# Kernel optimization log

Measured on AMD Instinct MI355X. Metric: run time of the kernel, lower is better.

The kernel has to match this reference:

```python
import jax, jax.numpy as jnp
import numpy as np

NEG_SLOPE = 0.2

def setup_inputs() -> dict:
    key = jax.random.key(0)
    k1, k2, k3, k4, k5 = jax.random.split(key, 5)
    N_src, N_dst, E, H, D = 50000, 50000, 1600000, 8, 16
    return {
        "h_src": jax.random.normal(k1, (N_src, H * D), dtype=jnp.float32),
        "h_dst": jax.random.normal(k2, (N_dst, H * D), dtype=jnp.float32),
        "attn_l": jax.random.normal(k3, (1, H, D), dtype=jnp.float32),
        "src": jax.random.randint(k4, (E,), 0, N_src, dtype=jnp.int32),
        "dst": jax.random.randint(k5, (E,), 0, N_dst, dtype=jnp.int32),
    }

def reference(h_src, h_dst, attn_l, src, dst):
    N_dst = h_dst.shape[0]
    H, D = attn_l.shape[1], attn_l.shape[2]
    hs = h_src.reshape(-1, H, D)                       # [N_src, H, D]
    el = jnp.sum(hs * attn_l, axis=-1)                 # [N_src, H] per-node attn logit
    e = jax.nn.leaky_relu(el[src], NEG_SLOPE)          # [E, H] per-edge score
    # edge softmax over incoming edges of each dst node (stable)
    seg_max = jax.ops.segment_max(e, dst, num_segments=N_dst)   # [N_dst, H]
    ex = jnp.exp(e - seg_max[dst])                     # [E, H]
    denom = jax.ops.segment_sum(ex, dst, num_segments=N_dst)    # [N_dst, H]
    a = ex / denom[dst]                                # [E, H]
    # gather-multiply-scatter: u_mul_e then sum by dst
    m = hs[src] * a[:, :, None]                        # [E, H, D]
    out = jax.ops.segment_sum(m, dst, num_segments=N_dst)       # [N_dst, H, D]
    return out.reshape(N_dst, H * D)
```

## Files before the change

kernel.cpp:

```cpp
#include <hip/hip_runtime.h>

#define Hh 8
#define HD 128
#define NEG_SLOPE 0.2f
#define EPB 4096
#define CAP 12288


__device__ __forceinline__ unsigned bfr(float f) {
    unsigned u = __float_as_uint(f);
    return (u + 0x7fffu + ((u >> 16) & 1u)) >> 16;
}
__device__ __forceinline__ unsigned pk(float a, float b) { return bfr(a) | (bfr(b) << 16); }

__global__ void __launch_bounds__(1024)
k_sort(const int* __restrict__ src, const int* __restrict__ dst,
       unsigned* __restrict__ tmp, int* __restrict__ blen,
       int E, int nblk, int nbkt,
       const float* __restrict__ hs, const float* __restrict__ attn,
       float* __restrict__ ew, uint4* __restrict__ hsb, int nh_src) {
    int t = threadIdx.x;
    if ((int)blockIdx.x < nblk) {
        __shared__ int lh[256], cur[256];
        if (t < 256) lh[t] = 0;
        __syncthreads();
        int base = blockIdx.x * EPB;
        int cnt = E - base; if (cnt > EPB) cnt = EPB;
        int i = t * 4;
        int4 d, s;
        bool vec = (i + 3 < cnt);
        if (vec) {
            d = *(const int4*)(dst + base + i);
            s = *(const int4*)(src + base + i);
            atomicAdd(&lh[d.x >> 8], 1);
            atomicAdd(&lh[d.y >> 8], 1);
            atomicAdd(&lh[d.z >> 8], 1);
            atomicAdd(&lh[d.w >> 8], 1);
        } else {
            for (int e = i; e < cnt; ++e) atomicAdd(&lh[dst[base + e] >> 8], 1);
        }
        __syncthreads();
        if (t < 256) {
            int v = lh[t];
            cur[t] = atomicAdd(&blen[t * 16], v);
        }
        __syncthreads();
        if (vec) {
            int p;
            p = atomicAdd(&cur[d.x >> 8], 1);
            tmp[(size_t)(d.x >> 8) * CAP + p] = ((unsigned)(d.x & 255) << 16) | (unsigned)s.x;
            p = atomicAdd(&cur[d.y >> 8], 1);
            tmp[(size_t)(d.y >> 8) * CAP + p] = ((unsigned)(d.y & 255) << 16) | (unsigned)s.y;
            p = atomicAdd(&cur[d.z >> 8], 1);
            tmp[(size_t)(d.z >> 8) * CAP + p] = ((unsigned)(d.z & 255) << 16) | (unsigned)s.z;
            p = atomicAdd(&cur[d.w >> 8], 1);
            tmp[(size_t)(d.w >> 8) * CAP + p] = ((unsigned)(d.w & 255) << 16) | (unsigned)s.w;
        } else {
            for (int e = i; e < cnt; ++e) {
                int dd = dst[base + e];
                int p = atomicAdd(&cur[dd >> 8], 1);
                tmp[(size_t)(dd >> 8) * CAP + p] =
                    ((unsigned)(dd & 255) << 16) | (unsigned)src[base + e];
            }
        }
    } else {
        int i = ((int)blockIdx.x - nblk) * 1024 + t;
        if (i >= nh_src) return;
        int n = i >> 3, h = i & 7;
        const float4* a = (const float4*)(hs + (size_t)n * HD + h * 16);
        const float4* w = (const float4*)(attn + h * 16);
        float4 x0 = a[0], x1 = a[1], x2 = a[2], x3 = a[3];
        float4 w0 = w[0], w1 = w[1], w2 = w[2], w3 = w[3];
        float sv = x0.x * w0.x + x0.y * w0.y + x0.z * w0.z + x0.w * w0.w
                 + x1.x * w1.x + x1.y * w1.y + x1.z * w1.z + x1.w * w1.w
                 + x2.x * w2.x + x2.y * w2.y + x2.z * w2.z + x2.w * w2.w
                 + x3.x * w3.x + x3.y * w3.y + x3.z * w3.z + x3.w * w3.w;
        sv = (sv >= 0.f) ? sv : NEG_SLOPE * sv;
        ew[i] = __expf(sv);
        uint4 p0 = { pk(x0.x, x0.y), pk(x0.z, x0.w), pk(x1.x, x1.y), pk(x1.z, x1.w) };
        uint4 p1 = { pk(x2.x, x2.y), pk(x2.z, x2.w), pk(x3.x, x3.y), pk(x3.z, x3.w) };
        hsb[(size_t)n * 16 + h * 2]     = p0;
        hsb[(size_t)n * 16 + h * 2 + 1] = p1;
    }
}

__global__ void __launch_bounds__(1024)
k_b3(const unsigned* __restrict__ tmp, const int* __restrict__ blen,
     unsigned short* __restrict__ adj, int* __restrict__ row_ptr,
     int E, int nbkt, int ndst) {
    __shared__ unsigned seg[CAP];
    __shared__ int lh[256], sh[256], cur[256];
    __shared__ int base_s;
    int b = blockIdx.x, t = threadIdx.x;
    int nb = blen[b * 16];
    int bc = 0;
    if (t < 256) {
        bc = (t < nbkt) ? blen[t * 16] : 0;
        sh[t] = bc;
        lh[t] = 0;
    }
    __syncthreads();
    for (int off = 1; off < 256; off <<= 1) {
        int x = 0;
        if (t < 256 && t >= off) x = sh[t - off];
        __syncthreads();
        if (t < 256) sh[t] += x;
        __syncthreads();
    }
    if (t == b) base_s = sh[t] - bc;
    __syncthreads();
    int base_b = base_s;
    const unsigned* tp = tmp + (size_t)b * CAP;
    for (int j = t; j < nb; j += 1024) {
        unsigned w = tp[j];
        seg[j] = w;
        atomicAdd(&lh[(w >> 16) & 255], 1);
    }
    __syncthreads();
    int v = 0;
    if (t < 256) { v = lh[t]; sh[t] = v; }
    __syncthreads();
    for (int off = 1; off < 256; off <<= 1) {
        int x = 0;
        if (t < 256 && t >= off) x = sh[t - off];
        __syncthreads();
        if (t < 256) sh[t] += x;
        __syncthreads();
    }
    if (t < 256) {
        int start = base_b + sh[t] - v;
        cur[t] = start;
        int d = b * 256 + t;
        if (d < ndst) row_ptr[d] = start;
        if (b == 0 && t == 0) row_ptr[ndst] = E;
    }
    __syncthreads();
    for (int j = t; j < nb; j += 1024) {
        unsigned w = seg[j];
        int pos = atomicAdd(&cur[(w >> 16) & 255], 1);
        adj[pos] = (unsigned short)(w & 0xffff);
    }
}

#define ACC8(X, W) \
    a0.x += __uint_as_float((X).x << 16) * (W); \
    a0.y += __uint_as_float((X).x & 0xffff0000u) * (W); \
    a0.z += __uint_as_float((X).y << 16) * (W); \
    a0.w += __uint_as_float((X).y & 0xffff0000u) * (W); \
    a1.x += __uint_as_float((X).z << 16) * (W); \
    a1.y += __uint_as_float((X).z & 0xffff0000u) * (W); \
    a1.z += __uint_as_float((X).w << 16) * (W); \
    a1.w += __uint_as_float((X).w & 0xffff0000u) * (W);

__global__ void __launch_bounds__(128)
k_agg(const int* __restrict__ row_ptr, const unsigned short* __restrict__ adj,
      const uint4* __restrict__ hsb, const float* __restrict__ ew,
      float* __restrict__ out) {
    int d = blockIdx.x;
    int t = threadIdx.x;
    int j0 = row_ptr[d], j1 = row_ptr[d + 1];
    int q = t & 15;
    int slot = t >> 4;
    int h = q >> 1;

    float4 a0 = {0.f, 0.f, 0.f, 0.f}, a1 = {0.f, 0.f, 0.f, 0.f};
    float ws = 0.f;
    int j = j0 + slot;
    for (; j + 24 < j1; j += 32) {
        int s0 = adj[j], s1 = adj[j + 8], s2 = adj[j + 16], s3 = adj[j + 24];
        float w0 = ew[s0 * Hh + h], w1 = ew[s1 * Hh + h];
        float w2 = ew[s2 * Hh + h], w3 = ew[s3 * Hh + h];
        uint4 x0 = hsb[(size_t)s0 * 16 + q];
        uint4 x1 = hsb[(size_t)s1 * 16 + q];
        uint4 x2 = hsb[(size_t)s2 * 16 + q];
        uint4 x3 = hsb[(size_t)s3 * 16 + q];
        ACC8(x0, w0)
        ACC8(x1, w1)
        ACC8(x2, w2)
        ACC8(x3, w3)
        ws += w0 + w1 + w2 + w3;
    }
    for (; j < j1; j += 8) {
        int s0 = adj[j];
        float w0 = ew[s0 * Hh + h];
        uint4 x0 = hsb[(size_t)s0 * 16 + q];
        ACC8(x0, w0)
        ws += w0;
    }

#pragma unroll
    for (int off = 16; off <= 32; off <<= 1) {
        a0.x += __shfl_xor(a0.x, off, 64);
        a0.y += __shfl_xor(a0.y, off, 64);
        a0.z += __shfl_xor(a0.z, off, 64);
        a0.w += __shfl_xor(a0.w, off, 64);
        a1.x += __shfl_xor(a1.x, off, 64);
        a1.y += __shfl_xor(a1.y, off, 64);
        a1.z += __shfl_xor(a1.z, off, 64);
        a1.w += __shfl_xor(a1.w, off, 64);
        ws   += __shfl_xor(ws,   off, 64);
    }
    __shared__ float4 sp0[16], sp1[16];
    __shared__ float wsp[16];
    if (t >= 64 && t < 80) { sp0[q] = a0; sp1[q] = a1; wsp[q] = ws; }
    __syncthreads();
    if (t < 16) {
        float wt = ws + wsp[t];
        float r = (wt > 0.f) ? 1.0f / wt : 0.f;
        float4 o0 = sp0[t], o1 = sp1[t];
        o0.x = (a0.x + o0.x) * r; o0.y = (a0.y + o0.y) * r;
        o0.z = (a0.z + o0.z) * r; o0.w = (a0.w + o0.w) * r;
        o1.x = (a1.x + o1.x) * r; o1.y = (a1.y + o1.y) * r;
        o1.z = (a1.z + o1.z) * r; o1.w = (a1.w + o1.w) * r;
        float4* op = (float4*)(out + (size_t)d * HD + t * 8);
        op[0] = o0;
        op[1] = o1;
    }
}

extern "C" void kernel_launch(void* const* d_in, const int* in_sizes, int n_in,
                              void* d_out, int out_size, void* d_ws, size_t ws_size,
                              hipStream_t stream) {
    const float* h_src  = (const float*)d_in[0];
    const float* attn_l = (const float*)d_in[2];
    const int*   src    = (const int*)d_in[3];
    const int*   dst    = (const int*)d_in[4];
    float* out = (float*)d_out;

    const int N_src = in_sizes[0] / HD;
    const int N_dst = in_sizes[1] / HD;
    const int E     = in_sizes[3];
    const int NH_src = N_src * Hh;

    const int NBLK  = (E + EPB - 1) / EPB;
    const int NBKT  = (N_dst + 255) / 256;
    const int NB_EW = (NH_src + 1023) / 1024;

    unsigned short* hsb = (unsigned short*)d_ws;
    float* ew = (float*)(hsb + (size_t)N_src * HD);
    unsigned* tmp = (unsigned*)(ew + NH_src);
    unsigned short* adj = (unsigned short*)(tmp + (size_t)NBKT * CAP);
    int* blen    = (int*)(adj + (((size_t)E + 1) & ~(size_t)1));
    int* row_ptr = blen + 256 * 16;

    hipMemsetAsync(blen, 0, 256 * 16 * sizeof(int), stream);
    k_sort<<<NBLK + NB_EW, 1024, 0, stream>>>(src, dst, tmp, blen, E, NBLK, NBKT,
                                              h_src, attn_l, ew, (uint4*)hsb, NH_src);
    k_b3<<<NBKT, 1024, 0, stream>>>(tmp, blen, adj, row_ptr, E, NBKT, N_dst);
    k_agg<<<N_dst, 128, 0, stream>>>(row_ptr, adj, (const uint4*)hsb, ew, out);
}
```

Before: 194.6 us.

## Replace global-atomic bucket append with per-block local bucket sort and offset table

```diff
diff --git a/kernel.cpp b/kernel.cpp
--- a/kernel.cpp
+++ b/kernel.cpp
@@ -4,7 +4,7 @@
 #define HD 128
 #define NEG_SLOPE 0.2f
 #define EPB 4096
-#define CAP 12288
+#define GRS 197
 
 
 __device__ __forceinline__ unsigned bfr(float f) {
@@ -14,53 +14,69 @@
 __device__ __forceinline__ unsigned pk(float a, float b) { return bfr(a) | (bfr(b) << 16); }
 
 __global__ void __launch_bounds__(1024)
-k_sort(const int* __restrict__ src, const int* __restrict__ dst,
-       unsigned* __restrict__ tmp, int* __restrict__ blen,
-       int E, int nblk, int nbkt,
-       const float* __restrict__ hs, const float* __restrict__ attn,
-       float* __restrict__ ew, uint4* __restrict__ hsb, int nh_src) {
+k1(const int* __restrict__ src, const int* __restrict__ dst,
+   unsigned* __restrict__ tmp, unsigned short* __restrict__ ghs,
+   int* __restrict__ bktTot, int E, int nblk,
+   const float* __restrict__ hs, const float* __restrict__ attn,
+   float* __restrict__ ew, uint4* __restrict__ hsb, int nh_src) {
     int t = threadIdx.x;
     if ((int)blockIdx.x < nblk) {
+        __shared__ unsigned wbuf[EPB];
         __shared__ int lh[256], cur[256];
+        int blk = blockIdx.x;
+        int base = blk * EPB;
+        int cnt = E - base; if (cnt > EPB) cnt = EPB;
         if (t < 256) lh[t] = 0;
         __syncthreads();
-        int base = blockIdx.x * EPB;
-        int cnt = E - base; if (cnt > EPB) cnt = EPB;
         int i = t * 4;
-        int4 d, s;
         bool vec = (i + 3 < cnt);
         if (vec) {
-            d = *(const int4*)(dst + base + i);
-            s = *(const int4*)(src + base + i);
+            int4 d = *(const int4*)(dst + base + i);
+            int4 s = *(const int4*)(src + base + i);
+            uint4 w;
+            w.x = ((unsigned)d.x << 16) | (unsigned)s.x;
+            w.y = ((unsigned)d.y << 16) | (unsigned)s.y;
+            w.z = ((unsigned)d.z << 16) | (unsigned)s.z;
+            w.w = ((unsigned)d.w << 16) | (unsigned)s.w;
+            ((uint4*)wbuf)[t] = w;
             atomicAdd(&lh[d.x >> 8], 1);
             atomicAdd(&lh[d.y >> 8], 1);
             atomicAdd(&lh[d.z >> 8], 1);
             atomicAdd(&lh[d.w >> 8], 1);
         } else {
-            for (int e = i; e < cnt; ++e) atomicAdd(&lh[dst[base + e] >> 8], 1);
-        }
-        __syncthreads();
-        if (t < 256) {
-            int v = lh[t];
-            cur[t] = atomicAdd(&blen[t * 16], v);
-        }
+            for (int e = i; e < cnt; ++e) {
+                int d = dst[base + e];
+                wbuf[e] = ((unsigned)d << 16) | (unsigned)src[base + e];
+                atomicAdd(&lh[d >> 8], 1);
+            }
+        }
+        __syncthreads();
+        int v = 0;
+        if (t < 256) { v = lh[t]; cur[t] = v; }
+        __syncthreads();
+        for (int off = 1; off < 256; off <<= 1) {
+            int x = 0;
+            if (t < 256 && t >= off) x = cur[t - off];
+            __syncthreads();
+            if (t < 256) cur[t] += x;
+            __syncthreads();
+        }
+        if (t < GRS) ghs[(size_t)blk * GRS + t] = (unsigned short)(cur[t] - ((t < 256) ? v : 0));
+        if (t < 196 && v) atomicAdd(&bktTot[t], v);
+        if (t < 256) cur[t] -= v;
         __syncthreads();
         if (vec) {
+            uint4 w = ((uint4*)wbuf)[t];
             int p;
-            p = atomicAdd(&cur[d.x >> 8], 1);
-            tmp[(size_t)(d.x >> 8) * CAP + p] = ((unsigned)(d.x & 255) << 16) | (unsigned)s.x;
-            p = atomicAdd(&cur[d.y >> 8], 1);
-            tmp[(size_t)(d.y >> 8) * CAP + p] = ((unsigned)(d.y & 255) << 16) | (unsigned)s.y;
-            p = atomicAdd(&cur[d.z >> 8], 1);
-            tmp[(size_t)(d.z >> 8) * CAP + p] = ((unsigned)(d.z & 255) << 16) | (unsigned)s.z;
-            p = atomicAdd(&cur[d.w >> 8], 1);
-            tmp[(size_t)(d.w >> 8) * CAP + p] = ((unsigned)(d.w & 255) << 16) | (unsigned)s.w;
+            p = atomicAdd(&cur[w.x >> 24], 1); tmp[base + p] = w.x;
+            p = atomicAdd(&cur[w.y >> 24], 1); tmp[base + p] = w.y;
+            p = atomicAdd(&cur[w.z >> 24], 1); tmp[base + p] = w.z;
+            p = atomicAdd(&cur[w.w >> 24], 1); tmp[base + p] = w.w;
         } else {
             for (int e = i; e < cnt; ++e) {
-                int dd = dst[base + e];
-                int p = atomicAdd(&cur[dd >> 8], 1);
-                tmp[(size_t)(dd >> 8) * CAP + p] =
-                    ((unsigned)(dd & 255) << 16) | (unsigned)src[base + e];
+                unsigned w = wbuf[e];
+                int p = atomicAdd(&cur[w >> 24], 1);
+                tmp[base + p] = w;
             }
         }
     } else {
@@ -85,20 +101,24 @@
 }
 
 __global__ void __launch_bounds__(1024)
-k_b3(const unsigned* __restrict__ tmp, const int* __restrict__ blen,
-     unsigned short* __restrict__ adj, int* __restrict__ row_ptr,
-     int E, int nbkt, int ndst) {
-    __shared__ unsigned seg[CAP];
+k2(const unsigned* __restrict__ tmp, const unsigned short* __restrict__ ghs,
+   const int* __restrict__ bktTot, unsigned short* __restrict__ adj,
+   int* __restrict__ row_ptr, int E, int nblk, int nbkt, int ndst) {
     __shared__ int lh[256], sh[256], cur[256];
     __shared__ int base_s;
     int b = blockIdx.x, t = threadIdx.x;
-    int nb = blen[b * 16];
+    if (t < 256) lh[t] = 0;
+    __syncthreads();
+    for (int blk = t; blk < nblk; blk += 1024) {
+        const unsigned short* gr = ghs + (size_t)blk * GRS;
+        int st = gr[b], en = gr[b + 1];
+        const unsigned* tp = tmp + (size_t)blk * EPB;
+        for (int j = st; j < en; ++j)
+            atomicAdd(&lh[(tp[j] >> 16) & 255], 1);
+    }
+    __syncthreads();
     int bc = 0;
-    if (t < 256) {
-        bc = (t < nbkt) ? blen[t * 16] : 0;
-        sh[t] = bc;
-        lh[t] = 0;
-    }
+    if (t < 256) { bc = (t < nbkt) ? bktTot[t] : 0; sh[t] = bc; }
     __syncthreads();
     for (int off = 1; off < 256; off <<= 1) {
         int x = 0;
@@ -110,13 +130,6 @@
     if (t == b) base_s = sh[t] - bc;
     __syncthreads();
     int base_b = base_s;
-    const unsigned* tp = tmp + (size_t)b * CAP;
-    for (int j = t; j < nb; j += 1024) {
-        unsigned w = tp[j];
-        seg[j] = w;
-        atomicAdd(&lh[(w >> 16) & 255], 1);
-    }
-    __syncthreads();
     int v = 0;
     if (t < 256) { v = lh[t]; sh[t] = v; }
     __syncthreads();
@@ -135,10 +148,15 @@
         if (b == 0 && t == 0) row_ptr[ndst] = E;
     }
     __syncthreads();
-    for (int j = t; j < nb; j += 1024) {
-        unsigned w = seg[j];
-        int pos = atomicAdd(&cur[(w >> 16) & 255], 1);
-        adj[pos] = (unsigned short)(w & 0xffff);
+    for (int blk = t; blk < nblk; blk += 1024) {
+        const unsigned short* gr = ghs + (size_t)blk * GRS;
+        int st = gr[b], en = gr[b + 1];
+        const unsigned* tp = tmp + (size_t)blk * EPB;
+        for (int j = st; j < en; ++j) {
+            unsigned w = tp[j];
+            int pos = atomicAdd(&cur[(w >> 16) & 255], 1);
+            adj[pos] = (unsigned short)(w & 0xffff);
+        }
     }
 }
 
@@ -239,13 +257,15 @@
     unsigned short* hsb = (unsigned short*)d_ws;
     float* ew = (float*)(hsb + (size_t)N_src * HD);
     unsigned* tmp = (unsigned*)(ew + NH_src);
-    unsigned short* adj = (unsigned short*)(tmp + (size_t)NBKT * CAP);
-    int* blen    = (int*)(adj + (((size_t)E + 1) & ~(size_t)1));
-    int* row_ptr = blen + 256 * 16;
-
-    hipMemsetAsync(blen, 0, 256 * 16 * sizeof(int), stream);
-    k_sort<<<NBLK + NB_EW, 1024, 0, stream>>>(src, dst, tmp, blen, E, NBLK, NBKT,
-                                              h_src, attn_l, ew, (uint4*)hsb, NH_src);
-    k_b3<<<NBKT, 1024, 0, stream>>>(tmp, blen, adj, row_ptr, E, NBKT, N_dst);
+    unsigned short* adj = (unsigned short*)(tmp + (size_t)NBLK * EPB);
+    unsigned short* ghs = adj + (((size_t)E + 1) & ~(size_t)1);
+    int* bktTot  = (int*)(ghs + (((size_t)NBLK * GRS + 1) & ~(size_t)1));
+    int* row_ptr = bktTot + 256;
+
+    hipMemsetAsync(bktTot, 0, 256 * sizeof(int), stream);
+    k1<<<NBLK + NB_EW, 1024, 0, stream>>>(src, dst, tmp, ghs, bktTot, E, NBLK,
+                                          h_src, attn_l, ew, (uint4*)hsb, NH_src);
+    k2<<<NBKT, 1024, 0, stream>>>(tmp, ghs, bktTot, adj, row_ptr,
+                                  E, NBLK, NBKT, N_dst);
     k_agg<<<N_dst, 128, 0, stream>>>(row_ptr, adj, (const uint4*)hsb, ew, out);
 }
```

Result: slower. 213.1 us (+9.5%).

## Split aggregation per destination across four blocks by feature quarter

Applied to the files above, without the earlier changes.

```diff
diff --git a/kernel.cpp b/kernel.cpp
--- a/kernel.cpp
+++ b/kernel.cpp
@@ -16,7 +16,7 @@
 __global__ void __launch_bounds__(1024)
 k_sort(const int* __restrict__ src, const int* __restrict__ dst,
        unsigned* __restrict__ tmp, int* __restrict__ blen,
-       int E, int nblk, int nbkt,
+       int E, int nblk,
        const float* __restrict__ hs, const float* __restrict__ attn,
        float* __restrict__ ew, uint4* __restrict__ hsb, int nh_src) {
     int t = threadIdx.x;
@@ -40,10 +40,7 @@
             for (int e = i; e < cnt; ++e) atomicAdd(&lh[dst[base + e] >> 8], 1);
         }
         __syncthreads();
-        if (t < 256) {
-            int v = lh[t];
-            cur[t] = atomicAdd(&blen[t * 16], v);
-        }
+        if (t < 256) cur[t] = atomicAdd(&blen[t * 16], lh[t]);
         __syncthreads();
         if (vec) {
             int p;
@@ -92,7 +89,7 @@
     __shared__ int lh[256], sh[256], cur[256];
     __shared__ int base_s;
     int b = blockIdx.x, t = threadIdx.x;
-    int nb = blen[b * 16];
+    int nb = blen[b * 16]; if (nb > CAP) nb = CAP;
     int bc = 0;
     if (t < 256) {
         bc = (t < nbkt) ? blen[t * 16] : 0;
@@ -142,7 +139,7 @@
     }
 }
 
-#define ACC8(X, W) \
+#define ACCQ(X, W) \
     a0.x += __uint_as_float((X).x << 16) * (W); \
     a0.y += __uint_as_float((X).x & 0xffff0000u) * (W); \
     a0.z += __uint_as_float((X).y << 16) * (W); \
@@ -153,43 +150,40 @@
     a1.w += __uint_as_float((X).w & 0xffff0000u) * (W);
 
 __global__ void __launch_bounds__(128)
-k_agg(const int* __restrict__ row_ptr, const unsigned short* __restrict__ adj,
-      const uint4* __restrict__ hsb, const float* __restrict__ ew,
-      float* __restrict__ out) {
+k_agg4(const int* __restrict__ row_ptr, const unsigned short* __restrict__ adj,
+       const uint4* __restrict__ hsb, const float* __restrict__ ew,
+       float* __restrict__ out) {
     int d = blockIdx.x;
+    int qtr = blockIdx.y;
     int t = threadIdx.x;
     int j0 = row_ptr[d], j1 = row_ptr[d + 1];
-    int q = t & 15;
-    int slot = t >> 4;
+    int qc = t & 3;
+    int slot = t >> 2;
+    int q = qtr * 4 + qc;
     int h = q >> 1;
 
     float4 a0 = {0.f, 0.f, 0.f, 0.f}, a1 = {0.f, 0.f, 0.f, 0.f};
     float ws = 0.f;
     int j = j0 + slot;
-    for (; j + 24 < j1; j += 32) {
-        int s0 = adj[j], s1 = adj[j + 8], s2 = adj[j + 16], s3 = adj[j + 24];
+    for (; j + 32 < j1; j += 64) {
+        int s0 = adj[j], s1 = adj[j + 32];
         float w0 = ew[s0 * Hh + h], w1 = ew[s1 * Hh + h];
-        float w2 = ew[s2 * Hh + h], w3 = ew[s3 * Hh + h];
         uint4 x0 = hsb[(size_t)s0 * 16 + q];
         uint4 x1 = hsb[(size_t)s1 * 16 + q];
-        uint4 x2 = hsb[(size_t)s2 * 16 + q];
-        uint4 x3 = hsb[(size_t)s3 * 16 + q];
-        ACC8(x0, w0)
-        ACC8(x1, w1)
-        ACC8(x2, w2)
-        ACC8(x3, w3)
-        ws += w0 + w1 + w2 + w3;
-    }
-    for (; j < j1; j += 8) {
+        ACCQ(x0, w0)
+        ACCQ(x1, w1)
+        ws += w0 + w1;
+    }
+    for (; j < j1; j += 32) {
         int s0 = adj[j];
         float w0 = ew[s0 * Hh + h];
         uint4 x0 = hsb[(size_t)s0 * 16 + q];
-        ACC8(x0, w0)
+        ACCQ(x0, w0)
         ws += w0;
     }
 
 #pragma unroll
-    for (int off = 16; off <= 32; off <<= 1) {
+    for (int off = 4; off <= 32; off <<= 1) {
         a0.x += __shfl_xor(a0.x, off, 64);
         a0.y += __shfl_xor(a0.y, off, 64);
         a0.z += __shfl_xor(a0.z, off, 64);
@@ -200,11 +194,11 @@
         a1.w += __shfl_xor(a1.w, off, 64);
         ws   += __shfl_xor(ws,   off, 64);
     }
-    __shared__ float4 sp0[16], sp1[16];
-    __shared__ float wsp[16];
-    if (t >= 64 && t < 80) { sp0[q] = a0; sp1[q] = a1; wsp[q] = ws; }
-    __syncthreads();
-    if (t < 16) {
+    __shared__ float4 sp0[4], sp1[4];
+    __shared__ float wsp[4];
+    if (t >= 64 && t < 68) { sp0[qc] = a0; sp1[qc] = a1; wsp[qc] = ws; }
+    __syncthreads();
+    if (t < 4) {
         float wt = ws + wsp[t];
         float r = (wt > 0.f) ? 1.0f / wt : 0.f;
         float4 o0 = sp0[t], o1 = sp1[t];
@@ -212,7 +206,7 @@
         o0.z = (a0.z + o0.z) * r; o0.w = (a0.w + o0.w) * r;
         o1.x = (a1.x + o1.x) * r; o1.y = (a1.y + o1.y) * r;
         o1.z = (a1.z + o1.z) * r; o1.w = (a1.w + o1.w) * r;
-        float4* op = (float4*)(out + (size_t)d * HD + t * 8);
+        float4* op = (float4*)(out + (size_t)d * HD + q * 8);
         op[0] = o0;
         op[1] = o1;
     }
@@ -240,12 +234,13 @@
     float* ew = (float*)(hsb + (size_t)N_src * HD);
     unsigned* tmp = (unsigned*)(ew + NH_src);
     unsigned short* adj = (unsigned short*)(tmp + (size_t)NBKT * CAP);
-    int* blen    = (int*)(adj + (((size_t)E + 1) & ~(size_t)1));
+    int* blen = (int*)(adj + (((size_t)E + 1) & ~(size_t)1));
     int* row_ptr = blen + 256 * 16;
 
     hipMemsetAsync(blen, 0, 256 * 16 * sizeof(int), stream);
-    k_sort<<<NBLK + NB_EW, 1024, 0, stream>>>(src, dst, tmp, blen, E, NBLK, NBKT,
+    k_sort<<<NBLK + NB_EW, 1024, 0, stream>>>(src, dst, tmp, blen, E, NBLK,
                                               h_src, attn_l, ew, (uint4*)hsb, NH_src);
     k_b3<<<NBKT, 1024, 0, stream>>>(tmp, blen, adj, row_ptr, E, NBKT, N_dst);
-    k_agg<<<N_dst, 128, 0, stream>>>(row_ptr, adj, (const uint4*)hsb, ew, out);
-}
+    dim3 gagg(N_dst, 4);
+    k_agg4<<<gagg, 128, 0, stream>>>(row_ptr, adj, (const uint4*)hsb, ew, out);
+}
```

After: 295.5 us. 1.52x slower.
